# Kernel optimization log

Measured on AMD Instinct MI355X. Metric: run time of the kernel, lower is better.

The kernel has to match this reference:

```python
import jax, jax.numpy as jnp
import numpy as np

NUM_CHIPS = 4
EXPERTS_PER_CHIP = 8
N_EXPERTS = 32            # NUM_CHIPS * EXPERTS_PER_CHIP
TOP_K = 4
SEQ = 1024
HIDDEN = 2048
MAX_TOK = 1024            # max_dispatched_tokens_per_expert
META_LEN = 8


def setup_inputs() -> dict:
    key = jax.random.key(0)
    k1, k2, k3 = jax.random.split(key, 3)
    x = jax.random.normal(k1, (NUM_CHIPS, SEQ, HIDDEN), jnp.float32)
    weights = jax.random.uniform(k2, (NUM_CHIPS, SEQ, TOP_K), jnp.float32)
    indices = jax.random.randint(k3, (NUM_CHIPS, SEQ, TOP_K), 0, N_EXPERTS, jnp.int32)
    return {"x": x, "weights": weights, "indices": indices}


def _dispatch_plan(indices):
    """Compute, for every (chip, token, topk) assignment, its destination slot in the
    global per-expert buffers, replicating the serialized offset-counter loop:
    chips write in order chip0..chipC, and within a chip in (token, topk) order."""
    C, S, K = indices.shape
    N = S * K
    e = indices.reshape(C, N)                                     # expert per assignment
    # per-chip per-expert counts
    counts = jax.vmap(lambda ec: jnp.zeros(N_EXPERTS, jnp.int32).at[ec].add(1))(e)  # [C,E]
    # exclusive prefix sum over chips -> starting offset of each chip within each expert buffer
    chip_off = jnp.cumsum(counts, axis=0) - counts                # [C,E]

    def rank_within_chip(ec, cnt):
        # stable sort groups assignments by expert while preserving (token, topk) order
        order = jnp.argsort(ec, stable=True)
        group_start = (jnp.cumsum(cnt) - cnt)[ec[order]]
        rk_sorted = jnp.arange(N, dtype=jnp.int32) - group_start
        return jnp.zeros(N, jnp.int32).at[order].set(rk_sorted)

    rank = jax.vmap(rank_within_chip)(e, counts)                  # [C,N]
    dst = jnp.take_along_axis(chip_off, e, axis=1) + rank         # slot within expert buffer
    flat = (e * MAX_TOK + dst).reshape(-1)                        # index into (E*MAX_TOK)
    return e, flat, counts


def reference(x, weights, indices):
    C, S, H = x.shape
    K = indices.shape[-1]
    N = S * K
    e, flat, counts = _dispatch_plan(indices)

    # scatter token vectors: each assignment gets a unique slot -> plain set
    x_rep = jnp.repeat(x, K, axis=1).reshape(C * N, H)
    buf = jnp.zeros((N_EXPERTS * MAX_TOK, H), x.dtype).at[flat].set(x_rep)
    buf = buf.reshape(NUM_CHIPS, EXPERTS_PER_CHIP, MAX_TOK, H)

    # metadata: [chip, token, topk, routed_expert, bf16-bits(weight), 0...]
    chip_id = jnp.broadcast_to(jnp.arange(C, dtype=jnp.int32)[:, None], (C, N))
    tok = jnp.broadcast_to(jnp.repeat(jnp.arange(S, dtype=jnp.int32), K)[None, :], (C, N))
    topk = jnp.broadcast_to(jnp.tile(jnp.arange(K, dtype=jnp.int32), S)[None, :], (C, N))
    wbits = jax.lax.bitcast_convert_type(weights.astype(jnp.bfloat16), jnp.int16)
    wbits = wbits.astype(jnp.int32).reshape(C, N)
    md = jnp.stack([chip_id, tok, topk, e, wbits], axis=-1)       # [C,N,5]
    md = jnp.concatenate([md, jnp.zeros((C, N, META_LEN - 5), jnp.int32)], axis=-1)
    meta = jnp.full((N_EXPERTS * MAX_TOK, META_LEN), -1, jnp.int32).at[flat].set(md.reshape(-1, META_LEN))
    meta = meta.reshape(NUM_CHIPS, EXPERTS_PER_CHIP, MAX_TOK, META_LEN)

    experts_counter = counts.sum(axis=0).reshape(NUM_CHIPS, EXPERTS_PER_CHIP)
    return buf, meta, experts_counter
```

## Files before the change

kernel.cpp:

```cpp
#include <hip/hip_runtime.h>
#include <hip/hip_bf16.h>
#include <stdint.h>
#include <string.h>

#define NUM_CHIPS 4
#define N_EXPERTS 32
#define TOP_K 4
#define SEQ 1024
#define HIDDEN 2048
#define MAX_TOK 1024
#define META_LEN 8
#define NPC (SEQ * TOP_K)
#define NTOT (NUM_CHIPS * NPC)
#define ROWS (N_EXPERTS * MAX_TOK)
#define BUF_ELEMS ((size_t)ROWS * HIDDEN)
#define META_OFF BUF_ELEMS
#define CNT_OFF (BUF_ELEMS + (size_t)ROWS * META_LEN)

#define WS_RANK 0
#define WS_CNT  (NTOT)

#define OCC_BLOCKS (NUM_CHIPS * SEQ)
#define EMPTY_BLOCKS (ROWS / 4)

typedef float vfloat4 __attribute__((ext_vector_type(4)));

__global__ __launch_bounds__(1024) void rank_kernel(const int* __restrict__ idx,
                                                    int* __restrict__ ws) {
    __shared__ int run_base[N_EXPERTS];
    __shared__ int wave_cnt[16][N_EXPERTS];
    __shared__ int wave_base[16][N_EXPERTS];

    const int c = blockIdx.x;
    const int t = threadIdx.x;
    const int lane = t & 63;
    const int w = t >> 6;

    int e[4];
#pragma unroll
    for (int q = 0; q < 4; ++q) e[q] = idx[c * NPC + q * 1024 + t];

    if (t < N_EXPERTS) run_base[t] = 0;
    __syncthreads();

#pragma unroll
    for (int q = 0; q < 4; ++q) {
        if (t < 16 * N_EXPERTS) ((int*)wave_cnt)[t] = 0;
        __syncthreads();

        uint64_t m = ~0ull;
#pragma unroll
        for (int b = 0; b < 5; ++b) {
            uint64_t bb = __ballot((e[q] >> b) & 1);
            m &= ((e[q] >> b) & 1) ? bb : ~bb;
        }
        const int rk = __popcll(m & ((1ull << lane) - 1ull));
        if (rk == 0) wave_cnt[w][e[q]] = __popcll(m);
        __syncthreads();

        if (t < N_EXPERTS) {
            int s = run_base[t];
#pragma unroll
            for (int ww = 0; ww < 16; ++ww) {
                wave_base[ww][t] = s;
                s += wave_cnt[ww][t];
            }
            run_base[t] = s;
        }
        __syncthreads();

        ws[WS_RANK + c * NPC + q * 1024 + t] = wave_base[w][e[q]] + rk;
    }
    __syncthreads();
    if (t < N_EXPERTS) ws[WS_CNT + c * N_EXPERTS + t] = run_base[t];
}

__global__ __launch_bounds__(256) void scatter_all(const float* __restrict__ x,
                                                   const float* __restrict__ wts,
                                                   const int* __restrict__ idx,
                                                   const int* __restrict__ ws,
                                                   float* __restrict__ out) {
    __shared__ int cnt_s[NUM_CHIPS * N_EXPERTS];
    const int t = threadIdx.x;
    const int b = blockIdx.x;

    if (b < OCC_BLOCKS) {
        const int c = b >> 10;
        const int tk = b & (SEQ - 1);

        if (t < NUM_CHIPS * N_EXPERTS) cnt_s[t] = ws[WS_CNT + t];

        const vfloat4* src = (const vfloat4*)(x + ((size_t)c * SEQ + tk) * HIDDEN);
        vfloat4 v0 = src[t];
        vfloat4 v1 = src[t + 256];

        int e[TOP_K], rk[TOP_K];
#pragma unroll
        for (int k = 0; k < TOP_K; ++k) {
            e[k] = idx[c * NPC + tk * TOP_K + k];
            rk[k] = ws[WS_RANK + c * NPC + tk * TOP_K + k];
        }
        __syncthreads();

#pragma unroll
        for (int k = 0; k < TOP_K; ++k) {
            int off = 0;
            for (int cc = 0; cc < c; ++cc) off += cnt_s[cc * N_EXPERTS + e[k]];
            const int row = e[k] * MAX_TOK + off + rk[k];

            vfloat4* dst = (vfloat4*)(out + (size_t)row * HIDDEN);
            dst[t] = v0;
            dst[t + 256] = v1;

            if (t < META_LEN) {
                float mv = 0.0f;
                if (t == 0) mv = (float)c;
                else if (t == 1) mv = (float)tk;
                else if (t == 2) mv = (float)k;
                else if (t == 3) mv = (float)e[k];
                else if (t == 4) {
                    float wv = wts[c * NPC + tk * TOP_K + k];
                    uint32_t ub;
                    memcpy(&ub, &wv, 4);
                    uint32_t lsb = (ub >> 16) & 1u;
                    uint32_t bits = (ub + 0x7FFFu + lsb) >> 16;
                    mv = (float)(int)(short)(uint16_t)bits;
                }
                out[META_OFF + (size_t)row * META_LEN + t] = mv;
            }
        }
    } else {
        const int row0 = (b - OCC_BLOCKS) * 4;
        const int e = row0 >> 10;
        const int slot0 = row0 & (MAX_TOK - 1);

        const int tot = ws[WS_CNT + e] + ws[WS_CNT + N_EXPERTS + e] +
                        ws[WS_CNT + 2 * N_EXPERTS + e] + ws[WS_CNT + 3 * N_EXPERTS + e];

        if (b == OCC_BLOCKS && t < N_EXPERTS) {
            int s = ws[WS_CNT + t] + ws[WS_CNT + N_EXPERTS + t] +
                    ws[WS_CNT + 2 * N_EXPERTS + t] + ws[WS_CNT + 3 * N_EXPERTS + t];
            out[CNT_OFF + t] = (float)s;
        }

        if (slot0 + 3 < tot) return;

        const vfloat4 z = (vfloat4)(0.f);
#pragma unroll
        for (int r = 0; r < 4; ++r) {
            if (slot0 + r < tot) continue;
            vfloat4* dst = (vfloat4*)(out + (size_t)(row0 + r) * HIDDEN);
            dst[t] = z;
            dst[t + 256] = z;
            if (t < META_LEN)
                out[META_OFF + (size_t)(row0 + r) * META_LEN + t] = -1.0f;
        }
    }
}

extern "C" void kernel_launch(void* const* d_in, const int* in_sizes, int n_in,
                              void* d_out, int out_size, void* d_ws, size_t ws_size,
                              hipStream_t stream) {
    const float* x   = (const float*)d_in[0];
    const float* wts = (const float*)d_in[1];
    const int*   idx = (const int*)d_in[2];
    float* out = (float*)d_out;
    int* ws = (int*)d_ws;

    rank_kernel<<<NUM_CHIPS, 1024, 0, stream>>>(idx, ws);
    scatter_all<<<OCC_BLOCKS + EMPTY_BLOCKS, 256, 0, stream>>>(x, wts, idx, ws, out);
}
```

Baseline: 296.1 us.

## Replace push-scatter with inverse map and per-destination-row gather writer

Adds a kernel that builds an inverse map from each destination row to its source (chip, assignment), then a writer kernel with one block per output row that gathers the source token or writes zeros and -1 metadata. The old design had each token block read its vector once and write it to four scattered rows, alongside separate zero-fill blocks. The new design writes output rows in sequential block order, which may give better write locality. In exchange it adds a third kernel launch and re-reads each x row up to four times, which is extra read traffic that caches may absorb.

```diff
diff --git a/kernel.cpp b/kernel.cpp
--- a/kernel.cpp
+++ b/kernel.cpp
@@ -19,9 +19,7 @@
 
 #define WS_RANK 0
 #define WS_CNT  (NTOT)
-
-#define OCC_BLOCKS (NUM_CHIPS * SEQ)
-#define EMPTY_BLOCKS (ROWS / 4)
+#define WS_INV  (NTOT + NUM_CHIPS * N_EXPERTS)
 
 typedef float vfloat4 __attribute__((ext_vector_type(4)));
 
@@ -75,86 +73,82 @@
     if (t < N_EXPERTS) ws[WS_CNT + c * N_EXPERTS + t] = run_base[t];
 }
 
-__global__ __launch_bounds__(256) void scatter_all(const float* __restrict__ x,
-                                                   const float* __restrict__ wts,
-                                                   const int* __restrict__ idx,
-                                                   const int* __restrict__ ws,
-                                                   float* __restrict__ out) {
+__global__ __launch_bounds__(1024) void inv_fill(const int* __restrict__ idx,
+                                                 int* __restrict__ ws) {
     __shared__ int cnt_s[NUM_CHIPS * N_EXPERTS];
     const int t = threadIdx.x;
-    const int b = blockIdx.x;
+    const int i = blockIdx.x * 1024 + t;
 
-    if (b < OCC_BLOCKS) {
-        const int c = b >> 10;
-        const int tk = b & (SEQ - 1);
+    if (t < NUM_CHIPS * N_EXPERTS) cnt_s[t] = ws[WS_CNT + t];
+    __syncthreads();
 
-        if (t < NUM_CHIPS * N_EXPERTS) cnt_s[t] = ws[WS_CNT + t];
+    const int c = i >> 12;
+    const int n = i & (NPC - 1);
+    const int e = idx[i];
+    const int rk = ws[WS_RANK + i];
+
+    int off = 0;
+    for (int cc = 0; cc < c; ++cc) off += cnt_s[cc * N_EXPERTS + e];
+    const int row = e * MAX_TOK + off + rk;
+
+    ws[WS_INV + row] = (c << 12) | n;
+}
+
+__global__ __launch_bounds__(256) void writer(const float* __restrict__ x,
+                                              const float* __restrict__ wts,
+                                              const int* __restrict__ ws,
+                                              float* __restrict__ out) {
+    const int t = threadIdx.x;
+    const int row = blockIdx.x;
+    const int e = row >> 10;
+    const int slot = row & (MAX_TOK - 1);
+
+    const int tot = ws[WS_CNT + e] + ws[WS_CNT + N_EXPERTS + e] +
+                    ws[WS_CNT + 2 * N_EXPERTS + e] + ws[WS_CNT + 3 * N_EXPERTS + e];
+
+    if (row == 0 && t < N_EXPERTS) {
+        int s = ws[WS_CNT + t] + ws[WS_CNT + N_EXPERTS + t] +
+                ws[WS_CNT + 2 * N_EXPERTS + t] + ws[WS_CNT + 3 * N_EXPERTS + t];
+        out[CNT_OFF + t] = (float)s;
+    }
+
+    vfloat4* dst = (vfloat4*)(out + (size_t)row * HIDDEN);
+
+    if (slot < tot) {
+        const int v = ws[WS_INV + row];
+        const int c = v >> 12;
+        const int n = v & (NPC - 1);
+        const int tk = n >> 2;
+        const int k = n & 3;
 
         const vfloat4* src = (const vfloat4*)(x + ((size_t)c * SEQ + tk) * HIDDEN);
-        vfloat4 v0 = src[t];
-        vfloat4 v1 = src[t + 256];
+        vfloat4 a = src[t];
+        vfloat4 b = src[t + 256];
+        dst[t] = a;
+        dst[t + 256] = b;
 
-        int e[TOP_K], rk[TOP_K];
-#pragma unroll
-        for (int k = 0; k < TOP_K; ++k) {
-            e[k] = idx[c * NPC + tk * TOP_K + k];
-            rk[k] = ws[WS_RANK + c * NPC + tk * TOP_K + k];
-        }
-        __syncthreads();
-
-#pragma unroll
-        for (int k = 0; k < TOP_K; ++k) {
-            int off = 0;
-            for (int cc = 0; cc < c; ++cc) off += cnt_s[cc * N_EXPERTS + e[k]];
-            const int row = e[k] * MAX_TOK + off + rk[k];
-
-            vfloat4* dst = (vfloat4*)(out + (size_t)row * HIDDEN);
-            dst[t] = v0;
-            dst[t + 256] = v1;
-
-            if (t < META_LEN) {
-                float mv = 0.0f;
-                if (t == 0) mv = (float)c;
-                else if (t == 1) mv = (float)tk;
-                else if (t == 2) mv = (float)k;
-                else if (t == 3) mv = (float)e[k];
-                else if (t == 4) {
-                    float wv = wts[c * NPC + tk * TOP_K + k];
-                    uint32_t ub;
-                    memcpy(&ub, &wv, 4);
-                    uint32_t lsb = (ub >> 16) & 1u;
-                    uint32_t bits = (ub + 0x7FFFu + lsb) >> 16;
-                    mv = (float)(int)(short)(uint16_t)bits;
-                }
-                out[META_OFF + (size_t)row * META_LEN + t] = mv;
+        if (t < META_LEN) {
+            float mv = 0.0f;
+            if (t == 0) mv = (float)c;
+            else if (t == 1) mv = (float)tk;
+            else if (t == 2) mv = (float)k;
+            else if (t == 3) mv = (float)e;
+            else if (t == 4) {
+                float wv = wts[(c << 12) + n];
+                uint32_t ub;
+                memcpy(&ub, &wv, 4);
+                uint32_t lsb = (ub >> 16) & 1u;
+                uint32_t bits = (ub + 0x7FFFu + lsb) >> 16;
+                mv = (float)(int)(short)(uint16_t)bits;
             }
+            out[META_OFF + (size_t)row * META_LEN + t] = mv;
         }
     } else {
-        const int row0 = (b - OCC_BLOCKS) * 4;
-        const int e = row0 >> 10;
-        const int slot0 = row0 & (MAX_TOK - 1);
-
-        const int tot = ws[WS_CNT + e] + ws[WS_CNT + N_EXPERTS + e] +
-                        ws[WS_CNT + 2 * N_EXPERTS + e] + ws[WS_CNT + 3 * N_EXPERTS + e];
-
-        if (b == OCC_BLOCKS && t < N_EXPERTS) {
-            int s = ws[WS_CNT + t] + ws[WS_CNT + N_EXPERTS + t] +
-                    ws[WS_CNT + 2 * N_EXPERTS + t] + ws[WS_CNT + 3 * N_EXPERTS + t];
-            out[CNT_OFF + t] = (float)s;
-        }
-
-        if (slot0 + 3 < tot) return;
-
         const vfloat4 z = (vfloat4)(0.f);
-#pragma unroll
-        for (int r = 0; r < 4; ++r) {
-            if (slot0 + r < tot) continue;
-            vfloat4* dst = (vfloat4*)(out + (size_t)(row0 + r) * HIDDEN);
-            dst[t] = z;
-            dst[t + 256] = z;
-            if (t < META_LEN)
-                out[META_OFF + (size_t)(row0 + r) * META_LEN + t] = -1.0f;
-        }
+        dst[t] = z;
+        dst[t + 256] = z;
+        if (t < META_LEN)
+            out[META_OFF + (size_t)row * META_LEN + t] = -1.0f;
     }
 }
 
@@ -168,5 +162,6 @@
     int* ws = (int*)d_ws;
 
     rank_kernel<<<NUM_CHIPS, 1024, 0, stream>>>(idx, ws);
-    scatter_all<<<OCC_BLOCKS + EMPTY_BLOCKS, 256, 0, stream>>>(x, wts, idx, ws, out);
+    inv_fill<<<NTOT / 1024, 1024, 0, stream>>>(idx, ws);
+    writer<<<ROWS, 256, 0, stream>>>(x, wts, ws, out);
 }
```

New measurement: 302.2 us. +2.1%, slower.
